# Performance work log

Hardware: AMD Instinct MI355X
Metric: run time of the kernel (lower is better)

## Reference

```python
import jax, jax.numpy as jnp
import numpy as np

N_NODES = 100000
N_EDGES = 3200000
D_IN = 128
D_OUT = 128


def setup_inputs() -> dict:
    key = jax.random.key(0)
    ks = jax.random.split(key, 7)
    x = jax.random.normal(ks[0], (N_NODES, D_IN), dtype=jnp.float32)
    weight = jax.random.normal(ks[1], (D_IN, D_OUT), dtype=jnp.float32) * (1.0 / np.sqrt(D_OUT))
    bias = jax.random.normal(ks[2], (D_OUT,), dtype=jnp.float32) * (1.0 / np.sqrt(D_OUT))
    adj_rows = jax.random.randint(ks[3], (N_EDGES,), 0, N_NODES, dtype=jnp.int32)
    adj_cols = jax.random.randint(ks[4], (N_EDGES,), 0, N_NODES, dtype=jnp.int32)
    adj_vals = jax.random.uniform(ks[5], (N_EDGES,), dtype=jnp.float32)
    # norm kept in [0.5, 1.5) to avoid division blow-up (degree-like normalizer)
    norm = jax.random.uniform(ks[6], (N_NODES, 1), dtype=jnp.float32) + 0.5
    return {"x": x, "weight": weight, "bias": bias,
            "adj_rows": adj_rows, "adj_cols": adj_cols, "adj_vals": adj_vals,
            "norm": norm}


def reference(x, weight, bias, adj_rows, adj_cols, adj_vals, norm):
    # support = input @ W               [N, D_OUT]
    support = x @ weight
    # output = spmm(adj, support): gather source rows, scale by edge value,
    # scatter-add into destination rows.
    gathered = support[adj_cols] * adj_vals[:, None]          # [E, D_OUT]
    output = jax.ops.segment_sum(gathered, adj_rows, num_segments=x.shape[0])
    output = output / norm
    return output + bias
```

## Files before the change

kernel.cpp:

```cpp
#include <hip/hip_runtime.h>

#define M_NODES 100000
#define N_EDGES 3200000
#define D 128
#define NBUCK 1563
#define FILL_CHUNK 12288
#define FILL_BLOCKS 261
#define GEMM_BLOCKS 1563
#define PREP_BLOCKS (FILL_BLOCKS + GEMM_BLOCKS)
#define BUCK_CAP 4096

#define OFF_SUP16  0ull
#define OFF_BCNT   25600000ull
#define OFF_REC    25608192ull
#define WS_NEEDED  76824576ull

typedef __attribute__((ext_vector_type(8))) short short8;
typedef __attribute__((ext_vector_type(4))) float f32x4;

__device__ __forceinline__ unsigned short f2bf(float f) {
    unsigned u = __float_as_uint(f);
    u += 0x7fff + ((u >> 16) & 1);
    return (unsigned short)(u >> 16);
}
__device__ __forceinline__ float bf2f(unsigned short h) {
    return __uint_as_float((unsigned)h << 16);
}
__device__ __forceinline__ float2 bfpair(unsigned u) {
    float2 r;
    r.x = __uint_as_float(u << 16);
    r.y = __uint_as_float(u & 0xffff0000u);
    return r;
}

__global__ __launch_bounds__(512) void prep_kernel(const float* __restrict__ x,
                                                   const float* __restrict__ w,
                                                   unsigned* __restrict__ sup16,
                                                   const int* __restrict__ rows,
                                                   const int* __restrict__ cols,
                                                   const float* __restrict__ vals,
                                                   int* __restrict__ bcnt,
                                                   int2* __restrict__ rec,
                                                   int M) {
    __shared__ __align__(16) char smem[37120];
    const int tid = threadIdx.x;

    if (blockIdx.x < FILL_BLOCKS) {
        int* cnt = (int*)smem;
        int* bas = (int*)(smem + 6256);
        unsigned short* lrank = (unsigned short*)(smem + 12512);
        for (int i = tid; i < NBUCK; i += 512) cnt[i] = 0;
        __syncthreads();
        const long long base = (long long)blockIdx.x * FILL_CHUNK;

#pragma unroll
        for (int i = 0; i < 6; ++i) {
            const int li = (i * 512 + tid) * 4;
            const long long e = base + li;
            if (e < N_EDGES) {
                const int4 r = *(const int4*)&rows[e];
                lrank[li + 0] = (unsigned short)atomicAdd(&cnt[r.x >> 6], 1);
                lrank[li + 1] = (unsigned short)atomicAdd(&cnt[r.y >> 6], 1);
                lrank[li + 2] = (unsigned short)atomicAdd(&cnt[r.z >> 6], 1);
                lrank[li + 3] = (unsigned short)atomicAdd(&cnt[r.w >> 6], 1);
            }
        }
        __syncthreads();
        for (int i = tid; i < NBUCK; i += 512)
            bas[i] = cnt[i] ? atomicAdd(&bcnt[i], cnt[i]) : 0;
        __syncthreads();
#pragma unroll
        for (int i = 0; i < 6; ++i) {
            const int li = (i * 512 + tid) * 4;
            const long long e = base + li;
            if (e < N_EDGES) {
                const int4   r = *(const int4*)&rows[e];
                const int4   c = *(const int4*)&cols[e];
                const float4 v = *(const float4*)&vals[e];
                int p;
                p = bas[r.x >> 6] + lrank[li + 0];
                if (p < BUCK_CAP)
                    rec[(size_t)(r.x >> 6) * BUCK_CAP + p] =
                        make_int2(c.x | ((r.x & 63) << 20), __float_as_int(v.x));
                p = bas[r.y >> 6] + lrank[li + 1];
                if (p < BUCK_CAP)
                    rec[(size_t)(r.y >> 6) * BUCK_CAP + p] =
                        make_int2(c.y | ((r.y & 63) << 20), __float_as_int(v.y));
                p = bas[r.z >> 6] + lrank[li + 2];
                if (p < BUCK_CAP)
                    rec[(size_t)(r.z >> 6) * BUCK_CAP + p] =
                        make_int2(c.z | ((r.z & 63) << 20), __float_as_int(v.z));
                p = bas[r.w >> 6] + lrank[li + 3];
                if (p < BUCK_CAP)
                    rec[(size_t)(r.w >> 6) * BUCK_CAP + p] =
                        make_int2(c.w | ((r.w & 63) << 20), __float_as_int(v.w));
            }
        }
        return;
    }

    short* xh = (short*)smem;
    short* xl = (short*)(smem + 5120);
    short* wh = (short*)(smem + 10240);
    short* wl = (short*)(smem + 20480);

    const int r0   = (blockIdx.x - FILL_BLOCKS) * 64;
    const int wv   = tid >> 6;
    const int lane = tid & 63;
    const int g    = lane >> 4;
    const int ml   = lane & 15;

    const int mt = wv & 3;
    const int ng = (wv >> 2) * 4;

    f32x4 acc[4];
#pragma unroll
    for (int i = 0; i < 4; ++i) acc[i] = (f32x4){0.f, 0.f, 0.f, 0.f};

    for (int c0 = 0; c0 < 128; c0 += 32) {
        {
            const int r  = tid >> 3;
            const int k0 = (tid & 7) * 4;
            float4 v = make_float4(0.f, 0.f, 0.f, 0.f);
            if (r0 + r < M)
                v = *(const float4*)&x[(size_t)(r0 + r) * D + c0 + k0];
            unsigned short h0 = f2bf(v.x), h1 = f2bf(v.y),
                           h2 = f2bf(v.z), h3 = f2bf(v.w);
            unsigned short l0 = f2bf(v.x - bf2f(h0)), l1 = f2bf(v.y - bf2f(h1)),
                           l2 = f2bf(v.z - bf2f(h2)), l3 = f2bf(v.w - bf2f(h3));
            uint2 ph, pl;
            ph.x = (unsigned)h0 | ((unsigned)h1 << 16);
            ph.y = (unsigned)h2 | ((unsigned)h3 << 16);
            pl.x = (unsigned)l0 | ((unsigned)l1 << 16);
            pl.y = (unsigned)l2 | ((unsigned)l3 << 16);
            *(uint2*)&xh[r * 40 + k0] = ph;
            *(uint2*)&xl[r * 40 + k0] = pl;
        }
        {
            const int k    = tid >> 4;
            const int col0 = (tid & 15) * 8;
            const float4 a = *(const float4*)&w[(size_t)(c0 + k) * D + col0];
            const float4 bq = *(const float4*)&w[(size_t)(c0 + k) * D + col0 + 4];
            const float vv[8] = {a.x, a.y, a.z, a.w, bq.x, bq.y, bq.z, bq.w};
#pragma unroll
            for (int j = 0; j < 8; ++j) {
                const unsigned short h = f2bf(vv[j]);
                wh[(col0 + j) * 40 + k] = (short)h;
                wl[(col0 + j) * 40 + k] = (short)f2bf(vv[j] - bf2f(h));
            }
        }
        __syncthreads();

        const short8 a_hi = *(const short8*)&xh[(mt * 16 + ml) * 40 + g * 8];
        const short8 a_lo = *(const short8*)&xl[(mt * 16 + ml) * 40 + g * 8];
#pragma unroll
        for (int i = 0; i < 4; ++i) {
            const int col = (ng + i) * 16 + ml;
            const short8 b_hi = *(const short8*)&wh[col * 40 + g * 8];
            const short8 b_lo = *(const short8*)&wl[col * 40 + g * 8];
            acc[i] = __builtin_amdgcn_mfma_f32_16x16x32_bf16(a_hi, b_hi, acc[i], 0, 0, 0);
            acc[i] = __builtin_amdgcn_mfma_f32_16x16x32_bf16(a_lo, b_hi, acc[i], 0, 0, 0);
            acc[i] = __builtin_amdgcn_mfma_f32_16x16x32_bf16(a_hi, b_lo, acc[i], 0, 0, 0);
        }
        __syncthreads();
    }

#pragma unroll
    for (int i = 0; i < 4; ++i) {
#pragma unroll
        for (int reg = 0; reg < 4; ++reg) {
            const float mine  = acc[i][reg];
            const float other = __shfl_xor(mine, 1);
            if (!(lane & 1)) {
                const unsigned uo = (unsigned)f2bf(mine) | ((unsigned)f2bf(other) << 16);
                const int grow = r0 + mt * 16 + g * 4 + reg;
                if (grow < M) {
                    const int word = (wv >> 2) * 32 + i * 8 + (ml >> 1);
                    sup16[(size_t)grow * 64 + word] = uo;
                }
            }
        }
    }
}

__global__ __launch_bounds__(512) void gather_kernel(const unsigned* __restrict__ sup16,
                                                     const int* __restrict__ bcnt,
                                                     const int2* __restrict__ rec,
                                                     const float* __restrict__ norm,
                                                     const float* __restrict__ bias,
                                                     float* __restrict__ out) {
    __shared__ int2 elist[BUCK_CAP];
    __shared__ int cnt[64];
    __shared__ int rbase[65];
    const int tid = threadIdx.x;
    const int b   = blockIdx.x;

    if (tid < 64) cnt[tid] = 0;
    __syncthreads();
    const int n = min(bcnt[b], BUCK_CAP);
    const int2* __restrict__ recb = rec + (size_t)b * BUCK_CAP;

    for (int k = tid; k < n; k += 512)
        atomicAdd(&cnt[(recb[k].x >> 20) & 63], 1);
    __syncthreads();
    if (tid == 0) {
        int run = 0;
#pragma unroll
        for (int i = 0; i < 64; ++i) {
            rbase[i] = run;
            run += cnt[i];
        }
        rbase[64] = run;
    }
    __syncthreads();
    if (tid < 64) cnt[tid] = rbase[tid];
    __syncthreads();
    for (int k = tid; k < n; k += 512) {
        const int2 e = recb[k];
        const int p = atomicAdd(&cnt[(e.x >> 20) & 63], 1);
        elist[p] = make_int2(e.x & 0xFFFFF, e.y);
    }
    __syncthreads();

    const int w    = tid >> 6;
    const int lane = tid & 63;
    const unsigned* __restrict__ supl = sup16 + lane;
    const int fo = lane * 2;
    const float2 b2 = *(const float2*)&bias[fo];

#pragma unroll 1
    for (int rr = 0; rr < 8; ++rr) {
        const int rl  = w * 8 + rr;
        const int row = b * 64 + rl;
        if (row >= M_NODES) break;
        const int j0 = rbase[rl];
        const int j1 = rbase[rl + 1];
        float2 acc = make_float2(0.f, 0.f);
        int j = j0;
        for (; j + 8 <= j1; j += 8) {
            int2 e[8];
#pragma unroll
            for (int q = 0; q < 8; ++q) e[q] = elist[j + q];
            unsigned u[8];
#pragma unroll
            for (int q = 0; q < 8; ++q) u[q] = supl[(unsigned)e[q].x << 6];
#pragma unroll
            for (int q = 0; q < 8; ++q) {
                const float v = __int_as_float(e[q].y);
                const float2 p = bfpair(u[q]);
                acc.x = fmaf(p.x, v, acc.x);
                acc.y = fmaf(p.y, v, acc.y);
            }
        }
        for (; j + 2 <= j1; j += 2) {
            const int2 e0 = elist[j];
            const int2 e1 = elist[j + 1];
            const unsigned u0 = supl[(unsigned)e0.x << 6];
            const unsigned u1 = supl[(unsigned)e1.x << 6];
            const float2 p0 = bfpair(u0);
            const float2 p1 = bfpair(u1);
            const float v0 = __int_as_float(e0.y);
            const float v1 = __int_as_float(e1.y);
            acc.x = fmaf(p0.x, v0, acc.x);
            acc.y = fmaf(p0.y, v0, acc.y);
            acc.x = fmaf(p1.x, v1, acc.x);
            acc.y = fmaf(p1.y, v1, acc.y);
        }
        for (; j < j1; ++j) {
            const int2 e = elist[j];
            const unsigned u = supl[(unsigned)e.x << 6];
            const float v = __int_as_float(e.y);
            const float2 p = bfpair(u);
            acc.x = fmaf(p.x, v, acc.x);
            acc.y = fmaf(p.y, v, acc.y);
        }
        const float inv = 1.0f / norm[row];
        float2 o;
        o.x = fmaf(acc.x, inv, b2.x);
        o.y = fmaf(acc.y, inv, b2.y);
        *(float2*)&out[(size_t)row * D + fo] = o;
    }
}

__global__ __launch_bounds__(256) void gemm32_kernel(const float* __restrict__ x,
                                                     const float* __restrict__ w,
                                                     float* __restrict__ support,
                                                     int M) {
    __shared__ float sX[32][64];
    __shared__ float sW[32][128];
    const int tid = threadIdx.x;
    const int r0  = blockIdx.x * 64;
    const int tx  = tid & 31;
    const int ty  = tid >> 5;
    float acc[8][4];
#pragma unroll
    for (int r = 0; r < 8; ++r)
#pragma unroll
        for (int c = 0; c < 4; ++c) acc[r][c] = 0.f;
    for (int c0 = 0; c0 < 128; c0 += 32) {
        {
            const int row = tid >> 3;
            const int kk  = (tid & 7) * 4;
#pragma unroll
            for (int h = 0; h < 2; ++h) {
                const int rr = row + h * 32;
                float4 v = make_float4(0.f, 0.f, 0.f, 0.f);
                if (r0 + rr < M)
                    v = *(const float4*)&x[(size_t)(r0 + rr) * D + c0 + kk];
                sX[kk + 0][rr] = v.x; sX[kk + 1][rr] = v.y;
                sX[kk + 2][rr] = v.z; sX[kk + 3][rr] = v.w;
            }
        }
#pragma unroll
        for (int i = tid; i < 1024; i += 256) {
            const int k  = i >> 5;
            const int c4 = (i & 31) * 4;
            *(float4*)&sW[k][c4] = *(const float4*)&w[(size_t)(c0 + k) * D + c4];
        }
        __syncthreads();
#pragma unroll
        for (int k = 0; k < 32; ++k) {
            const float4 wv = *(const float4*)&sW[k][tx * 4];
            const float4 xa = *(const float4*)&sX[k][ty * 8];
            const float4 xb = *(const float4*)&sX[k][ty * 8 + 4];
            const float xr[8] = {xa.x, xa.y, xa.z, xa.w, xb.x, xb.y, xb.z, xb.w};
#pragma unroll
            for (int r = 0; r < 8; ++r) {
                acc[r][0] += xr[r] * wv.x; acc[r][1] += xr[r] * wv.y;
                acc[r][2] += xr[r] * wv.z; acc[r][3] += xr[r] * wv.w;
            }
        }
        __syncthreads();
    }
#pragma unroll
    for (int r = 0; r < 8; ++r) {
        const int row = r0 + ty * 8 + r;
        if (row < M)
            *(float4*)&support[(size_t)row * D + tx * 4] =
                make_float4(acc[r][0], acc[r][1], acc[r][2], acc[r][3]);
    }
}

__global__ __launch_bounds__(256) void spmm_kernel(const float* __restrict__ support,
                                                   const int* __restrict__ rows,
                                                   const int* __restrict__ cols,
                                                   const float* __restrict__ vals,
                                                   float* __restrict__ out) {
    const long long t = (long long)blockIdx.x * 256 + threadIdx.x;
    const int e = (int)(t >> 5);
    if (e >= N_EDGES) return;
    const int f   = (int)(t & 31) * 4;
    const int src = cols[e];
    const int dst = rows[e];
    const float v = vals[e];
    const float4 s = *(const float4*)&support[(size_t)src * D + f];
    float* o = &out[(size_t)dst * D + f];
    atomicAdd(o + 0, s.x * v);
    atomicAdd(o + 1, s.y * v);
    atomicAdd(o + 2, s.z * v);
    atomicAdd(o + 3, s.w * v);
}

__global__ __launch_bounds__(256) void finalize_kernel(float* __restrict__ out,
                                                       const float* __restrict__ norm,
                                                       const float* __restrict__ bias) {
    const int t = blockIdx.x * 256 + threadIdx.x;
    const int nrow = t >> 5;
    if (nrow >= M_NODES) return;
    const int f = (t & 31) * 4;
    const float inv = 1.0f / norm[nrow];
    float4 o = *(float4*)&out[(size_t)nrow * D + f];
    const float4 b = *(const float4*)&bias[f];
    o.x = o.x * inv + b.x; o.y = o.y * inv + b.y;
    o.z = o.z * inv + b.z; o.w = o.w * inv + b.w;
    *(float4*)&out[(size_t)nrow * D + f] = o;
}

extern "C" void kernel_launch(void* const* d_in, const int* in_sizes, int n_in,
                              void* d_out, int out_size, void* d_ws, size_t ws_size,
                              hipStream_t stream) {
    const float* x    = (const float*)d_in[0];
    const float* w    = (const float*)d_in[1];
    const float* bias = (const float*)d_in[2];
    const int*   rows = (const int*)d_in[3];
    const int*   cols = (const int*)d_in[4];
    const float* vals = (const float*)d_in[5];
    const float* norm = (const float*)d_in[6];
    float* out = (float*)d_out;
    char* ws = (char*)d_ws;

    if (ws_size >= WS_NEEDED) {
        unsigned* sup16 = (unsigned*)(ws + OFF_SUP16);
        int*      bcnt  = (int*)(ws + OFF_BCNT);
        int2*     rec   = (int2*)(ws + OFF_REC);

        hipMemsetAsync(bcnt, 0, NBUCK * sizeof(int), stream);
        prep_kernel<<<PREP_BLOCKS, 512, 0, stream>>>(x, w, sup16, rows, cols, vals,
                                                     bcnt, rec, M_NODES);
        gather_kernel<<<NBUCK, 512, 0, stream>>>(sup16, bcnt, rec,
                                                 norm, bias, out);
    } else {
        float* support = (float*)ws;
        gemm32_kernel<<<(M_NODES + 63) / 64, 256, 0, stream>>>(x, w, support, M_NODES);
        hipMemsetAsync(d_out, 0, (size_t)out_size * sizeof(float), stream);
        const long long spmm_threads = (long long)N_EDGES * 32;
        spmm_kernel<<<(int)((spmm_threads + 255) / 256), 256, 0, stream>>>(support, rows, cols, vals, out);
        finalize_kernel<<<(M_NODES * 32 + 255) / 256, 256, 0, stream>>>(out, norm, bias);
    }
}
```

Measured before the change: 317.4 us.

## Sort bucket edges by source-range segment so waves gather across eight rows together

The bucket sort key now combines a coarse source-node segment (source id >> 14, seven segments) with the destination row. Each wave walks all eight of its rows together within each source segment, keeping eight accumulators and picking the target with a wave-uniform switch. The aim is to make gathers from the bf16 support table hit a narrower address range at a time, improving cache locality. In exchange it adds a 512-entry parallel prefix scan with many barriers, switch dispatch on every edge, and more registers.

```diff
diff --git a/kernel.cpp b/kernel.cpp
--- a/kernel.cpp
+++ b/kernel.cpp
@@ -9,6 +9,7 @@
 #define GEMM_BLOCKS 1563
 #define PREP_BLOCKS (FILL_BLOCKS + GEMM_BLOCKS)
 #define BUCK_CAP 4096
+#define NSEG 7
 
 #define OFF_SUP16  0ull
 #define OFF_BCNT   25600000ull
@@ -190,35 +191,42 @@
                                                      const float* __restrict__ bias,
                                                      float* __restrict__ out) {
     __shared__ int2 elist[BUCK_CAP];
-    __shared__ int cnt[64];
-    __shared__ int rbase[65];
+    __shared__ int cnt[512];
+    __shared__ int rbase[514];
     const int tid = threadIdx.x;
     const int b   = blockIdx.x;
 
-    if (tid < 64) cnt[tid] = 0;
+    cnt[tid] = 0;
     __syncthreads();
     const int n = min(bcnt[b], BUCK_CAP);
     const int2* __restrict__ recb = rec + (size_t)b * BUCK_CAP;
 
-    for (int k = tid; k < n; k += 512)
-        atomicAdd(&cnt[(recb[k].x >> 20) & 63], 1);
+    for (int k = tid; k < n; k += 512) {
+        const int ex = recb[k].x;
+        const int key = (((ex & 0xFFFFF) >> 14) << 6) | ((ex >> 20) & 63);
+        atomicAdd(&cnt[key], 1);
+    }
     __syncthreads();
-    if (tid == 0) {
-        int run = 0;
-#pragma unroll
-        for (int i = 0; i < 64; ++i) {
-            rbase[i] = run;
-            run += cnt[i];
-        }
-        rbase[64] = run;
-    }
+    int* tsum = (int*)elist;
+    const int myc = cnt[tid];
+    tsum[tid] = myc;
     __syncthreads();
-    if (tid < 64) cnt[tid] = rbase[tid];
+    for (int off = 1; off < 512; off <<= 1) {
+        const int v = (tid >= off) ? tsum[tid - off] : 0;
+        __syncthreads();
+        tsum[tid] += v;
+        __syncthreads();
+    }
+    const int excl = tsum[tid] - myc;
+    rbase[tid] = excl;
+    cnt[tid]   = excl;
+    if (tid == 0) rbase[512] = n;
     __syncthreads();
     for (int k = tid; k < n; k += 512) {
         const int2 e = recb[k];
-        const int p = atomicAdd(&cnt[(e.x >> 20) & 63], 1);
-        elist[p] = make_int2(e.x & 0xFFFFF, e.y);
+        const int key = (((e.x & 0xFFFFF) >> 14) << 6) | ((e.x >> 20) & 63);
+        const int p = atomicAdd(&cnt[key], 1);
+        elist[p] = e;
     }
     __syncthreads();
 
@@ -228,57 +236,66 @@
     const int fo = lane * 2;
     const float2 b2 = *(const float2*)&bias[fo];
 
+    float2 acc[8];
+#pragma unroll
+    for (int r = 0; r < 8; ++r) acc[r] = make_float2(0.f, 0.f);
+
+#define GDISPATCH(EX, PX, PY, VV)                                         \
+    {                                                                     \
+        const int rl_ = (__builtin_amdgcn_readfirstlane(EX) >> 20) & 7;   \
+        switch (rl_) {                                                    \
+        case 0: acc[0].x = fmaf(PX, VV, acc[0].x); acc[0].y = fmaf(PY, VV, acc[0].y); break; \
+        case 1: acc[1].x = fmaf(PX, VV, acc[1].x); acc[1].y = fmaf(PY, VV, acc[1].y); break; \
+        case 2: acc[2].x = fmaf(PX, VV, acc[2].x); acc[2].y = fmaf(PY, VV, acc[2].y); break; \
+        case 3: acc[3].x = fmaf(PX, VV, acc[3].x); acc[3].y = fmaf(PY, VV, acc[3].y); break; \
+        case 4: acc[4].x = fmaf(PX, VV, acc[4].x); acc[4].y = fmaf(PY, VV, acc[4].y); break; \
+        case 5: acc[5].x = fmaf(PX, VV, acc[5].x); acc[5].y = fmaf(PY, VV, acc[5].y); break; \
+        case 6: acc[6].x = fmaf(PX, VV, acc[6].x); acc[6].y = fmaf(PY, VV, acc[6].y); break; \
+        default: acc[7].x = fmaf(PX, VV, acc[7].x); acc[7].y = fmaf(PY, VV, acc[7].y); break; \
+        }                                                                 \
+    }
+
 #pragma unroll 1
-    for (int rr = 0; rr < 8; ++rr) {
-        const int rl  = w * 8 + rr;
-        const int row = b * 64 + rl;
-        if (row >= M_NODES) break;
-        const int j0 = rbase[rl];
-        const int j1 = rbase[rl + 1];
-        float2 acc = make_float2(0.f, 0.f);
-        int j = j0;
+    for (int seg = 0; seg < NSEG; ++seg) {
+        const int kb = seg * 64 + (w << 3);
+        int j        = __builtin_amdgcn_readfirstlane(rbase[kb]);
+        const int j1 = __builtin_amdgcn_readfirstlane(rbase[kb + 8]);
+#pragma unroll 1
         for (; j + 8 <= j1; j += 8) {
             int2 e[8];
 #pragma unroll
             for (int q = 0; q < 8; ++q) e[q] = elist[j + q];
             unsigned u[8];
 #pragma unroll
-            for (int q = 0; q < 8; ++q) u[q] = supl[(unsigned)e[q].x << 6];
+            for (int q = 0; q < 8; ++q)
+                u[q] = supl[(unsigned)(e[q].x & 0xFFFFF) << 6];
 #pragma unroll
             for (int q = 0; q < 8; ++q) {
-                const float v = __int_as_float(e[q].y);
+                const float vv = __int_as_float(e[q].y);
                 const float2 p = bfpair(u[q]);
-                acc.x = fmaf(p.x, v, acc.x);
-                acc.y = fmaf(p.y, v, acc.y);
-            }
-        }
-        for (; j + 2 <= j1; j += 2) {
-            const int2 e0 = elist[j];
-            const int2 e1 = elist[j + 1];
-            const unsigned u0 = supl[(unsigned)e0.x << 6];
-            const unsigned u1 = supl[(unsigned)e1.x << 6];
-            const float2 p0 = bfpair(u0);
-            const float2 p1 = bfpair(u1);
-            const float v0 = __int_as_float(e0.y);
-            const float v1 = __int_as_float(e1.y);
-            acc.x = fmaf(p0.x, v0, acc.x);
-            acc.y = fmaf(p0.y, v0, acc.y);
-            acc.x = fmaf(p1.x, v1, acc.x);
-            acc.y = fmaf(p1.y, v1, acc.y);
+                GDISPATCH(e[q].x, p.x, p.y, vv)
+            }
         }
         for (; j < j1; ++j) {
             const int2 e = elist[j];
-            const unsigned u = supl[(unsigned)e.x << 6];
-            const float v = __int_as_float(e.y);
-            const float2 p = bfpair(u);
-            acc.x = fmaf(p.x, v, acc.x);
-            acc.y = fmaf(p.y, v, acc.y);
-        }
-        const float inv = 1.0f / norm[row];
-        float2 o;
-        o.x = fmaf(acc.x, inv, b2.x);
-        o.y = fmaf(acc.y, inv, b2.y);
-        *(float2*)&out[(size_t)row * D + fo] = o;
+            const unsigned uu = supl[(unsigned)(e.x & 0xFFFFF) << 6];
+            const float vv = __int_as_float(e.y);
+            const float2 p = bfpair(uu);
+            GDISPATCH(e.x, p.x, p.y, vv)
+        }
+    }
+#undef GDISPATCH
+
+#pragma unroll
+    for (int rr = 0; rr < 8; ++rr) {
+        const int row = b * 64 + (w << 3) + rr;
+        if (row < M_NODES) {
+            const float inv = 1.0f / norm[row];
+            float2 o;
+            o.x = fmaf(acc[rr].x, inv, b2.x);
+            o.y = fmaf(acc[rr].y, inv, b2.y);
+            *(float2*)&out[(size_t)row * D + fo] = o;
+        }
     }
 }
 
```

Result: slower. 448.1 us (+41.2%).
